# Optimization experiments

Measured on AMD Instinct MI355X. Metric: run time of the kernel, lower is better.

Reference implementation:

```python
import jax, jax.numpy as jnp
import numpy as np

HIDDEN = 1024
HEADS = 16
HEAD_DIM = HIDDEN // HEADS  # 64; softmax scale uses head_dim per SeqAttention(hidden_size=head_dim)


def setup_inputs() -> dict:
    key = jax.random.key(0)
    ks = jax.random.split(key, 7)
    B, M = 2, 2048
    s = 1.0 / np.sqrt(HIDDEN)
    return {
        "query": jax.random.normal(ks[0], (B, M, HIDDEN), jnp.float32),
        "key": jax.random.normal(ks[1], (B, M, HIDDEN), jnp.float32),
        "value": jax.random.normal(ks[2], (B, M, HIDDEN), jnp.float32),
        "Wq": jax.random.normal(ks[3], (HIDDEN, HIDDEN), jnp.float32) * s,
        "Wk": jax.random.normal(ks[4], (HIDDEN, HIDDEN), jnp.float32) * s,
        "Wv": jax.random.normal(ks[5], (HIDDEN, HIDDEN), jnp.float32) * s,
        "Wo": jax.random.normal(ks[6], (HIDDEN, HIDDEN), jnp.float32) * s,
    }


def _split_heads(x):
    # [B, T, H*D] -> [B, H, T, D]
    B, T, _ = x.shape
    return x.reshape(B, T, HEADS, HEAD_DIM).transpose(0, 2, 1, 3)


def reference(query, key, value, Wq, Wk, Wv, Wo):
    # nn.Linear(bias=False): y = x @ W.T
    q = _split_heads(query @ Wq.T)  # [B,H,M,D]
    k = _split_heads(key @ Wk.T)    # [B,H,N,D]
    v = _split_heads(value @ Wv.T)  # [B,H,N,D]
    scale = 1.0 / jnp.sqrt(jnp.asarray(HEAD_DIM, q.dtype))
    attn = jnp.einsum("bhmd,bhnd->bhmn", q, k) * scale
    attn = jax.nn.softmax(attn, axis=-1)
    out = jnp.einsum("bhmn,bhnd->bhmd", attn, v)  # [B,H,M,D]
    B, H, M, D = out.shape
    out = out.transpose(0, 2, 1, 3).reshape(B, M, H * D)
    return out @ Wo.T
```

## Files before the change

kernel.cpp:

```cpp
#include <hip/hip_runtime.h>

typedef __bf16 bf16;
typedef __bf16 bf16x2 __attribute__((ext_vector_type(2)));
typedef __bf16 bf16x8 __attribute__((ext_vector_type(8)));
typedef float  f32x4  __attribute__((ext_vector_type(4)));
typedef float  f32x16 __attribute__((ext_vector_type(16)));
typedef unsigned int u32;
typedef unsigned int u32x4 __attribute__((ext_vector_type(4)));

typedef __attribute__((address_space(1))) unsigned int gu32;
typedef __attribute__((address_space(3))) unsigned int lu32;

__device__ __forceinline__ void llds16(const void* g, void* l) {
  __builtin_amdgcn_global_load_lds((gu32*)g, (lu32*)l, 16, 0, 0);
}

__device__ __forceinline__ void cvt8(const float* __restrict__ src,
                                     bf16* __restrict__ dst, int i) {
  const float4* s4 = (const float4*)src;
  float4 a = s4[i * 2 + 0];
  float4 c = s4[i * 2 + 1];
  bf16x8 o;
  o[0] = (bf16)a.x; o[1] = (bf16)a.y; o[2] = (bf16)a.z; o[3] = (bf16)a.w;
  o[4] = (bf16)c.x; o[5] = (bf16)c.y; o[6] = (bf16)c.z; o[7] = (bf16)c.w;
  ((bf16x8*)dst)[i] = o;
}

__global__ __launch_bounds__(256) void cvt_bf16(const float* __restrict__ src,
                                                bf16* __restrict__ dst, int n8) {
  int i = blockIdx.x * blockDim.x + threadIdx.x;
  if (i < n8) cvt8(src, dst, i);
}

__global__ __launch_bounds__(256) void cvt_all(const float* __restrict__ w0,
                                               const float* __restrict__ w1,
                                               const float* __restrict__ w2,
                                               const float* __restrict__ w3,
                                               const float* __restrict__ x0,
                                               const float* __restrict__ x1,
                                               const float* __restrict__ x2,
                                               bf16* __restrict__ wdst,
                                               bf16* __restrict__ xdst) {
  const int b = blockIdx.x;
  if (b < 2048) {
    const int which = b >> 9;
    const float* src = (which == 0) ? w0 : (which == 1) ? w1 : (which == 2) ? w2 : w3;
    const int i = (b & 511) * 256 + threadIdx.x;
    cvt8(src, wdst + (size_t)which * (1u << 20), i);
  } else {
    const int b2 = b - 2048;
    const int which = b2 >> 11;
    const float* src = (which == 0) ? x0 : (which == 1) ? x1 : x2;
    const int i = (b2 & 2047) * 256 + threadIdx.x;
    cvt8(src, xdst + (size_t)which * (4u << 20), i);
  }
}

__global__ __launch_bounds__(256) void gemm_qkv(const bf16* __restrict__ A0,
                                                const bf16* __restrict__ A1,
                                                const bf16* __restrict__ A2,
                                                const bf16* __restrict__ Wb,
                                                bf16* __restrict__ qb,
                                                bf16* __restrict__ kb,
                                                bf16* __restrict__ vb,
                                                int zoff) {
  constexpr int K = 1024, BM = 128, BN = 128, BK = 32, NT = K / BK;
  __shared__ bf16 Alds[2][BM * BK];
  __shared__ bf16 Blds[2][BN * BK];
  const int t = threadIdx.x, w = t >> 6, l = t & 63;
  const int lr = l & 15, lg = l >> 4;
  const int bm = blockIdx.x * BM, bn = blockIdx.y * BN;
  const int z = blockIdx.z + zoff;
  const bf16* A = (z == 0) ? A0 : (z == 1) ? A1 : A2;
  const bf16* W = Wb + (size_t)z * (1u << 20);
  const int wm = (w >> 1) * 64, wn = (w & 1) * 64;

  f32x4 acc[4][4] = {};

  auto stage = [&](int buf, int kt) {
    const int k0 = kt * BK;
#pragma unroll
    for (int i = 0; i < 2; ++i) {
      int idx = i * 256 + t;
      int row = idx >> 2, kb2 = (idx & 3) * 16;
      llds16((const char*)A + ((size_t)(bm + row) * K + k0) * 2 + kb2,
             (char*)(&Alds[buf][0]) + (i * 4 + w) * 1024);
    }
#pragma unroll
    for (int i = 0; i < 2; ++i) {
      int idx = i * 256 + t;
      int row = idx >> 2, kb2 = (idx & 3) * 16;
      llds16((const char*)W + ((size_t)(bn + row) * K + k0) * 2 + kb2,
             (char*)(&Blds[buf][0]) + (i * 4 + w) * 1024);
    }
  };

  stage(0, 0);
  for (int kt = 0; kt < NT; ++kt) {
    __syncthreads();
    if (kt + 1 < NT) stage((kt + 1) & 1, kt + 1);
    const int cur = kt & 1;
    bf16x8 af[4], bfr[4];
#pragma unroll
    for (int i = 0; i < 4; ++i)
      af[i] = *(const bf16x8*)(&Alds[cur][(wm + i * 16 + lr) * BK + lg * 8]);
#pragma unroll
    for (int j = 0; j < 4; ++j)
      bfr[j] = *(const bf16x8*)(&Blds[cur][(wn + j * 16 + lr) * BK + lg * 8]);
    __builtin_amdgcn_s_setprio(1);
#pragma unroll
    for (int i = 0; i < 4; ++i)
#pragma unroll
      for (int j = 0; j < 4; ++j)
        acc[i][j] = __builtin_amdgcn_mfma_f32_16x16x32_bf16(af[i], bfr[j], acc[i][j], 0, 0, 0);
    __builtin_amdgcn_s_setprio(0);
  }

  bf16* Cout = (z == 0) ? qb : (z == 1) ? kb : vb;
  const float osc = (z == 0) ? 0.1803368801f : 1.0f;
#pragma unroll
  for (int i = 0; i < 4; ++i) {
#pragma unroll
    for (int j = 0; j < 4; ++j) {
#pragma unroll
      for (int r = 0; r < 4; ++r) {
        const int gm = bm + wm + i * 16 + lg * 4 + r;
        const int n  = bn + wn + j * 16 + lr;
        const int b = gm >> 11, m = gm & 2047;
        const int h = n >> 6, d = n & 63;
        const size_t off = (z < 2)
            ? ((size_t)((b * 16 + h) * 2048 + m) * 64 + d)
            : ((size_t)((b * 16 + h) * 64 + d) * 2048 + m);
        Cout[off] = (bf16)(acc[i][j][r] * osc);
      }
    }
  }
}

__global__ __launch_bounds__(256) void gemm_out(const bf16* __restrict__ A,
                                                const bf16* __restrict__ Bw,
                                                float* __restrict__ Cout) {
  constexpr int N = 1024, K = 1024;
  constexpr int BM = 128, BN = 64, BK = 32;
  __shared__ bf16 Alds[2][BM * BK];
  __shared__ bf16 Blds[2][BN * BK];
  const int t = threadIdx.x;
  const int w = t >> 6, l = t & 63;
  const int lr = l & 15, lg = l >> 4;
  const int bm = blockIdx.x * BM, bn = blockIdx.y * BN;
  const int wm = (w >> 1) * 64, wn = (w & 1) * 32;

  f32x4 acc[4][2] = {};

  auto stage = [&](int buf, int kt) {
    const int k0 = kt * BK;
#pragma unroll
    for (int i = 0; i < 2; ++i) {
      int idx = i * 256 + t;
      int row = idx >> 2, kb = (idx & 3) * 16;
      const char* g = (const char*)A + ((size_t)(bm + row) * K + k0) * 2 + kb;
      llds16(g, (char*)(&Alds[buf][0]) + (i * 4 + w) * 1024);
    }
    {
      int row = t >> 2, kb = (t & 3) * 16;
      const char* g = (const char*)Bw + ((size_t)(bn + row) * K + k0) * 2 + kb;
      llds16(g, (char*)(&Blds[buf][0]) + w * 1024);
    }
  };

  stage(0, 0);
  constexpr int NT = K / BK;
  for (int kt = 0; kt < NT; ++kt) {
    __syncthreads();
    if (kt + 1 < NT) stage((kt + 1) & 1, kt + 1);
    const int cur = kt & 1;
    bf16x8 af[4], bfr[2];
#pragma unroll
    for (int i = 0; i < 4; ++i)
      af[i] = *(const bf16x8*)(&Alds[cur][(wm + i * 16 + lr) * BK + lg * 8]);
#pragma unroll
    for (int j = 0; j < 2; ++j)
      bfr[j] = *(const bf16x8*)(&Blds[cur][(wn + j * 16 + lr) * BK + lg * 8]);
    __builtin_amdgcn_s_setprio(1);
#pragma unroll
    for (int i = 0; i < 4; ++i)
#pragma unroll
      for (int j = 0; j < 2; ++j)
        acc[i][j] = __builtin_amdgcn_mfma_f32_16x16x32_bf16(af[i], bfr[j], acc[i][j], 0, 0, 0);
    __builtin_amdgcn_s_setprio(0);
  }

#pragma unroll
  for (int i = 0; i < 4; ++i)
#pragma unroll
    for (int j = 0; j < 2; ++j)
#pragma unroll
      for (int r = 0; r < 4; ++r) {
        const int gm = bm + wm + i * 16 + lg * 4 + r;
        const int n  = bn + wn + j * 16 + lr;
        Cout[(size_t)gm * N + n] = acc[i][j][r];
      }
}

__global__ __launch_bounds__(256) void attn_fwd(const bf16* __restrict__ Qb,
                                                const bf16* __restrict__ Kb,
                                                const bf16* __restrict__ Vt,
                                                bf16* __restrict__ Out) {
  constexpr int Mlen = 2048, KVB = 64, NTT = Mlen / KVB;
  __shared__ bf16 Klds[3][KVB * 64];
  __shared__ bf16 Vlds[3][64 * KVB];
  const int t = threadIdx.x, w = t >> 6, l = t & 63;
  const int l31 = l & 31, hi = l >> 5;
  const int orig = blockIdx.x;
  const int wg = (orig & 7) * 64 + (orig >> 3);
  const int bh = wg >> 4;
  const int qr = (wg & 15) * 128 + w * 32;
  const int key = (l31 & 7) << 4;

  const bf16* qbase = Qb + ((size_t)bh * Mlen + qr + l31) * 64;
  bf16x8 qf[4];
#pragma unroll
  for (int dks = 0; dks < 4; ++dks)
    qf[dks] = *(const bf16x8*)(qbase + dks * 16 + hi * 8);

  f32x16 acco0 = {}, acco1 = {};
  float lsum = 0.f;

  const char* kTile0 = (const char*)Kb + (size_t)bh * Mlen * 64 * 2;
  const char* vBase  = (const char*)Vt + (size_t)bh * 64 * Mlen * 2;

  auto stageKV = [&](int buf, int tile) {
    const int kv0 = tile * KVB;
#pragma unroll
    for (int i = 0; i < 2; ++i) {
      int idx = i * 256 + t;
      int L = idx * 16;
      int row = L >> 7;
      int inner = (L & 127) ^ ((row & 7) << 4);
      llds16(kTile0 + (size_t)(kv0 + row) * 128 + inner,
             (char*)(&Klds[buf][0]) + (i * 4 + w) * 1024);
    }
#pragma unroll
    for (int i = 0; i < 2; ++i) {
      int idx = i * 256 + t;
      int L = idx * 16;
      int d = L >> 7;
      int inner = (L & 127) ^ ((d & 7) << 4);
      llds16(vBase + (size_t)d * (Mlen * 2) + kv0 * 2 + inner,
             (char*)(&Vlds[buf][0]) + (i * 4 + w) * 1024);
    }
  };

  stageKV(0, 0);
  int bufc = 0;
  for (int tile = 0; tile < NTT; ++tile) {
    const int bufn = (bufc == 2) ? 0 : bufc + 1;
    if (tile + 1 < NTT) {
      stageKV(bufn, tile + 1);
      asm volatile("s_waitcnt vmcnt(4)" ::: "memory");
    } else {
      asm volatile("s_waitcnt vmcnt(0)" ::: "memory");
    }
    __builtin_amdgcn_s_barrier();
    __builtin_amdgcn_sched_barrier(0);
    const char* kb_ = (const char*)(&Klds[bufc][0]);
    const char* vb_ = (const char*)(&Vlds[bufc][0]);

    f32x16 s0 = {}, s1 = {};
    __builtin_amdgcn_s_setprio(1);
#pragma unroll
    for (int dks = 0; dks < 4; ++dks) {
      const int a0 = (0 * 32 + l31) * 128 + ((dks * 32 + hi * 16) ^ key);
      const int a1 = (1 * 32 + l31) * 128 + ((dks * 32 + hi * 16) ^ key);
      bf16x8 kf0 = *(const bf16x8*)(kb_ + a0);
      bf16x8 kf1 = *(const bf16x8*)(kb_ + a1);
      s0 = __builtin_amdgcn_mfma_f32_32x32x16_bf16(kf0, qf[dks], s0, 0, 0, 0);
      s1 = __builtin_amdgcn_mfma_f32_32x32x16_bf16(kf1, qf[dks], s1, 0, 0, 0);
    }
    __builtin_amdgcn_s_setprio(0);

    u32 wrd0[8], wrd1[8];
    float ts = 0.f;
#pragma unroll
    for (int e2 = 0; e2 < 8; ++e2) {
      const float p00 = __builtin_amdgcn_exp2f(s0[2 * e2]);
      const float p01 = __builtin_amdgcn_exp2f(s0[2 * e2 + 1]);
      const float p10 = __builtin_amdgcn_exp2f(s1[2 * e2]);
      const float p11 = __builtin_amdgcn_exp2f(s1[2 * e2 + 1]);
      ts += (p00 + p01) + (p10 + p11);
      bf16x2 k0; k0[0] = (bf16)p00; k0[1] = (bf16)p01;
      bf16x2 k1; k1[0] = (bf16)p10; k1[1] = (bf16)p11;
      wrd0[e2] = __builtin_bit_cast(u32, k0);
      wrd1[e2] = __builtin_bit_cast(u32, k1);
    }
    lsum += ts;

    __builtin_amdgcn_s_setprio(1);
#pragma unroll
    for (int ks = 0; ks < 2; ++ks) {
      auto sa0 = __builtin_amdgcn_permlane32_swap(wrd0[4 * ks + 0], wrd0[4 * ks + 2], false, false);
      auto sa1 = __builtin_amdgcn_permlane32_swap(wrd0[4 * ks + 1], wrd0[4 * ks + 3], false, false);
      auto sb0 = __builtin_amdgcn_permlane32_swap(wrd1[4 * ks + 0], wrd1[4 * ks + 2], false, false);
      auto sb1 = __builtin_amdgcn_permlane32_swap(wrd1[4 * ks + 1], wrd1[4 * ks + 3], false, false);
      u32x4 fa, fb;
      fa[0] = (u32)sa0[0]; fa[1] = (u32)sa1[0]; fa[2] = (u32)sa0[1]; fa[3] = (u32)sa1[1];
      fb[0] = (u32)sb0[0]; fb[1] = (u32)sb1[0]; fb[2] = (u32)sb0[1]; fb[3] = (u32)sb1[1];
      const bf16x8 pa = __builtin_bit_cast(bf16x8, fa);
      const bf16x8 pb = __builtin_bit_cast(bf16x8, fb);
      const int c0 = (ks * 32 + hi * 16);
      bf16x8 va0 = *(const bf16x8*)(vb_ + (0 * 32 + l31) * 128 + ((0 * 64 + c0) ^ key));
      bf16x8 va1 = *(const bf16x8*)(vb_ + (1 * 32 + l31) * 128 + ((0 * 64 + c0) ^ key));
      bf16x8 vb0 = *(const bf16x8*)(vb_ + (0 * 32 + l31) * 128 + ((1 * 64 + c0) ^ key));
      bf16x8 vb1 = *(const bf16x8*)(vb_ + (1 * 32 + l31) * 128 + ((1 * 64 + c0) ^ key));
      acco0 = __builtin_amdgcn_mfma_f32_32x32x16_bf16(pa, va0, acco0, 0, 0, 0);
      acco1 = __builtin_amdgcn_mfma_f32_32x32x16_bf16(pa, va1, acco1, 0, 0, 0);
      acco0 = __builtin_amdgcn_mfma_f32_32x32x16_bf16(pb, vb0, acco0, 0, 0, 0);
      acco1 = __builtin_amdgcn_mfma_f32_32x32x16_bf16(pb, vb1, acco1, 0, 0, 0);
    }
    __builtin_amdgcn_s_setprio(0);
    bufc = bufn;
  }

  float lf = lsum + __shfl_xor(lsum, 32, 64);
  const float inv = 1.0f / lf;
  const int b = bh >> 4, h = bh & 15;
#pragma unroll
  for (int e = 0; e < 16; ++e) {
    const int ql = (e & 3) + 8 * (e >> 2) + 4 * hi;
    const float iv = __shfl(inv, ql, 64);
    const size_t row = (size_t)(b * 2048 + qr + ql) * 1024 + h * 64;
    Out[row + l31]      = (bf16)(acco0[e] * iv);
    Out[row + 32 + l31] = (bf16)(acco1[e] * iv);
  }
}

extern "C" void kernel_launch(void* const* d_in, const int* in_sizes, int n_in,
                              void* d_out, int out_size, void* d_ws, size_t ws_size,
                              hipStream_t stream) {
  const float* q  = (const float*)d_in[0];
  const float* k  = (const float*)d_in[1];
  const float* v  = (const float*)d_in[2];
  const float* Wq = (const float*)d_in[3];
  const float* Wk = (const float*)d_in[4];
  const float* Wv = (const float*)d_in[5];
  const float* Wo = (const float*)d_in[6];

  char* ws = (char*)d_ws;
  const dim3 cb(256);

  if (ws_size >= ((size_t)56 << 20)) {
    bf16* Wb = (bf16*)ws;
    bf16* Xq = (bf16*)(ws + (8u  << 20));
    bf16* Xk = (bf16*)(ws + (16u << 20));
    bf16* Xv = (bf16*)(ws + (24u << 20));
    bf16* qb = (bf16*)(ws + (32u << 20));
    bf16* kb = (bf16*)(ws + (40u << 20));
    bf16* vb = (bf16*)(ws + (48u << 20));
    bf16* Xa = (bf16*)(ws + (8u  << 20));

    cvt_all<<<8192, cb, 0, stream>>>(Wq, Wk, Wv, Wo, q, k, v, Wb, Xq);
    gemm_qkv<<<dim3(32, 8, 3), cb, 0, stream>>>(Xq, Xk, Xv, Wb, qb, kb, vb, 0);
    attn_fwd<<<512, cb, 0, stream>>>(qb, kb, vb, Xa);
    gemm_out<<<dim3(32, 16), cb, 0, stream>>>(Xa, Wb + 3 * (1u << 20), (float*)d_out);
  } else {
    bf16* Wb = (bf16*)ws;
    bf16* X  = (bf16*)(ws + (8u  << 20));
    bf16* qb = (bf16*)(ws + (16u << 20));
    bf16* kb = (bf16*)(ws + (24u << 20));
    bf16* vb = (bf16*)(ws + (32u << 20));
    bf16* Xa = (bf16*)(ws + (8u  << 20));

    cvt_all<<<2048, cb, 0, stream>>>(Wq, Wk, Wv, Wo, q, k, v, Wb, Wb);
    cvt_bf16<<<2048, cb, 0, stream>>>(q, X, 524288);
    gemm_qkv<<<dim3(32, 8, 1), cb, 0, stream>>>(X, X, X, Wb, qb, kb, vb, 0);
    cvt_bf16<<<2048, cb, 0, stream>>>(k, X, 524288);
    gemm_qkv<<<dim3(32, 8, 1), cb, 0, stream>>>(X, X, X, Wb, qb, kb, vb, 1);
    cvt_bf16<<<2048, cb, 0, stream>>>(v, X, 524288);
    gemm_qkv<<<dim3(32, 8, 1), cb, 0, stream>>>(X, X, X, Wb, qb, kb, vb, 2);
    attn_fwd<<<512, cb, 0, stream>>>(qb, kb, vb, Xa);
    gemm_out<<<dim3(32, 16), cb, 0, stream>>>(Xa, Wb + 3 * (1u << 20), (float*)d_out);
  }
}
```

Before: 131.8 us.

## Widen output GEMM tile to 128x128 and compute softmax row sums via MFMA

The output projection GEMM moves from a 128x64 to a 128x128 block tile: each wave now holds a 4x4 set of accumulators and the grid is halved to 32x8 blocks. This increases reuse of A and B per LDS load but leaves fewer blocks to occupy the GPU. In attention, the per-lane scalar exp accumulation and the cross-lane shuffle of the row sum are replaced by an extra MFMA that multiplies P by a ones vector, so the row sums come out in the same layout as the output accumulator. This removes VALU adds and shuffles in exchange for two more MFMAs per iteration and 16 more accumulator registers. The row sums are now taken from the bf16-rounded probabilities rather than the fp32 values.

```diff
diff --git a/kernel.cpp b/kernel.cpp
--- a/kernel.cpp
+++ b/kernel.cpp
@@ -141,16 +141,16 @@
                                                 const bf16* __restrict__ Bw,
                                                 float* __restrict__ Cout) {
   constexpr int N = 1024, K = 1024;
-  constexpr int BM = 128, BN = 64, BK = 32;
+  constexpr int BM = 128, BN = 128, BK = 32, NT = K / BK;
   __shared__ bf16 Alds[2][BM * BK];
   __shared__ bf16 Blds[2][BN * BK];
   const int t = threadIdx.x;
   const int w = t >> 6, l = t & 63;
   const int lr = l & 15, lg = l >> 4;
   const int bm = blockIdx.x * BM, bn = blockIdx.y * BN;
-  const int wm = (w >> 1) * 64, wn = (w & 1) * 32;
-
-  f32x4 acc[4][2] = {};
+  const int wm = (w >> 1) * 64, wn = (w & 1) * 64;
+
+  f32x4 acc[4][4] = {};
 
   auto stage = [&](int buf, int kt) {
     const int k0 = kt * BK;
@@ -158,34 +158,35 @@
     for (int i = 0; i < 2; ++i) {
       int idx = i * 256 + t;
       int row = idx >> 2, kb = (idx & 3) * 16;
-      const char* g = (const char*)A + ((size_t)(bm + row) * K + k0) * 2 + kb;
-      llds16(g, (char*)(&Alds[buf][0]) + (i * 4 + w) * 1024);
-    }
-    {
-      int row = t >> 2, kb = (t & 3) * 16;
-      const char* g = (const char*)Bw + ((size_t)(bn + row) * K + k0) * 2 + kb;
-      llds16(g, (char*)(&Blds[buf][0]) + w * 1024);
+      llds16((const char*)A + ((size_t)(bm + row) * K + k0) * 2 + kb,
+             (char*)(&Alds[buf][0]) + (i * 4 + w) * 1024);
+    }
+#pragma unroll
+    for (int i = 0; i < 2; ++i) {
+      int idx = i * 256 + t;
+      int row = idx >> 2, kb = (idx & 3) * 16;
+      llds16((const char*)Bw + ((size_t)(bn + row) * K + k0) * 2 + kb,
+             (char*)(&Blds[buf][0]) + (i * 4 + w) * 1024);
     }
   };
 
   stage(0, 0);
-  constexpr int NT = K / BK;
   for (int kt = 0; kt < NT; ++kt) {
     __syncthreads();
     if (kt + 1 < NT) stage((kt + 1) & 1, kt + 1);
     const int cur = kt & 1;
-    bf16x8 af[4], bfr[2];
+    bf16x8 af[4], bfr[4];
 #pragma unroll
     for (int i = 0; i < 4; ++i)
       af[i] = *(const bf16x8*)(&Alds[cur][(wm + i * 16 + lr) * BK + lg * 8]);
 #pragma unroll
-    for (int j = 0; j < 2; ++j)
+    for (int j = 0; j < 4; ++j)
       bfr[j] = *(const bf16x8*)(&Blds[cur][(wn + j * 16 + lr) * BK + lg * 8]);
     __builtin_amdgcn_s_setprio(1);
 #pragma unroll
     for (int i = 0; i < 4; ++i)
 #pragma unroll
-      for (int j = 0; j < 2; ++j)
+      for (int j = 0; j < 4; ++j)
         acc[i][j] = __builtin_amdgcn_mfma_f32_16x16x32_bf16(af[i], bfr[j], acc[i][j], 0, 0, 0);
     __builtin_amdgcn_s_setprio(0);
   }
@@ -193,7 +194,7 @@
 #pragma unroll
   for (int i = 0; i < 4; ++i)
 #pragma unroll
-    for (int j = 0; j < 2; ++j)
+    for (int j = 0; j < 4; ++j)
 #pragma unroll
       for (int r = 0; r < 4; ++r) {
         const int gm = bm + wm + i * 16 + lg * 4 + r;
@@ -223,8 +224,13 @@
   for (int dks = 0; dks < 4; ++dks)
     qf[dks] = *(const bf16x8*)(qbase + dks * 16 + hi * 8);
 
+  u32x4 onesw;
+  onesw[0] = 0x3F803F80u; onesw[1] = 0x3F803F80u;
+  onesw[2] = 0x3F803F80u; onesw[3] = 0x3F803F80u;
+  const bf16x8 ones = __builtin_bit_cast(bf16x8, onesw);
+
   f32x16 acco0 = {}, acco1 = {};
-  float lsum = 0.f;
+  f32x16 accl = {};
 
   const char* kTile0 = (const char*)Kb + (size_t)bh * Mlen * 64 * 2;
   const char* vBase  = (const char*)Vt + (size_t)bh * 64 * Mlen * 2;
@@ -280,20 +286,17 @@
     __builtin_amdgcn_s_setprio(0);
 
     u32 wrd0[8], wrd1[8];
-    float ts = 0.f;
 #pragma unroll
     for (int e2 = 0; e2 < 8; ++e2) {
       const float p00 = __builtin_amdgcn_exp2f(s0[2 * e2]);
       const float p01 = __builtin_amdgcn_exp2f(s0[2 * e2 + 1]);
       const float p10 = __builtin_amdgcn_exp2f(s1[2 * e2]);
       const float p11 = __builtin_amdgcn_exp2f(s1[2 * e2 + 1]);
-      ts += (p00 + p01) + (p10 + p11);
       bf16x2 k0; k0[0] = (bf16)p00; k0[1] = (bf16)p01;
       bf16x2 k1; k1[0] = (bf16)p10; k1[1] = (bf16)p11;
       wrd0[e2] = __builtin_bit_cast(u32, k0);
       wrd1[e2] = __builtin_bit_cast(u32, k1);
     }
-    lsum += ts;
 
     __builtin_amdgcn_s_setprio(1);
 #pragma unroll
@@ -314,20 +317,20 @@
       bf16x8 vb1 = *(const bf16x8*)(vb_ + (1 * 32 + l31) * 128 + ((1 * 64 + c0) ^ key));
       acco0 = __builtin_amdgcn_mfma_f32_32x32x16_bf16(pa, va0, acco0, 0, 0, 0);
       acco1 = __builtin_amdgcn_mfma_f32_32x32x16_bf16(pa, va1, acco1, 0, 0, 0);
+      accl  = __builtin_amdgcn_mfma_f32_32x32x16_bf16(pa, ones, accl, 0, 0, 0);
       acco0 = __builtin_amdgcn_mfma_f32_32x32x16_bf16(pb, vb0, acco0, 0, 0, 0);
       acco1 = __builtin_amdgcn_mfma_f32_32x32x16_bf16(pb, vb1, acco1, 0, 0, 0);
+      accl  = __builtin_amdgcn_mfma_f32_32x32x16_bf16(pb, ones, accl, 0, 0, 0);
     }
     __builtin_amdgcn_s_setprio(0);
     bufc = bufn;
   }
 
-  float lf = lsum + __shfl_xor(lsum, 32, 64);
-  const float inv = 1.0f / lf;
   const int b = bh >> 4, h = bh & 15;
 #pragma unroll
   for (int e = 0; e < 16; ++e) {
     const int ql = (e & 3) + 8 * (e >> 2) + 4 * hi;
-    const float iv = __shfl(inv, ql, 64);
+    const float iv = 1.0f / accl[e];
     const size_t row = (size_t)(b * 2048 + qr + ql) * 1024 + h * 64;
     Out[row + l31]      = (bf16)(acco0[e] * iv);
     Out[row + 32 + l31] = (bf16)(acco1[e] * iv);
@@ -361,7 +364,7 @@
     cvt_all<<<8192, cb, 0, stream>>>(Wq, Wk, Wv, Wo, q, k, v, Wb, Xq);
     gemm_qkv<<<dim3(32, 8, 3), cb, 0, stream>>>(Xq, Xk, Xv, Wb, qb, kb, vb, 0);
     attn_fwd<<<512, cb, 0, stream>>>(qb, kb, vb, Xa);
-    gemm_out<<<dim3(32, 16), cb, 0, stream>>>(Xa, Wb + 3 * (1u << 20), (float*)d_out);
+    gemm_out<<<dim3(32, 8), cb, 0, stream>>>(Xa, Wb + 3 * (1u << 20), (float*)d_out);
   } else {
     bf16* Wb = (bf16*)ws;
     bf16* X  = (bf16*)(ws + (8u  << 20));
@@ -378,6 +381,6 @@
     cvt_bf16<<<2048, cb, 0, stream>>>(v, X, 524288);
     gemm_qkv<<<dim3(32, 8, 1), cb, 0, stream>>>(X, X, X, Wb, qb, kb, vb, 2);
     attn_fwd<<<512, cb, 0, stream>>>(qb, kb, vb, Xa);
-    gemm_out<<<dim3(32, 16), cb, 0, stream>>>(Xa, Wb + 3 * (1u << 20), (float*)d_out);
-  }
-}
+    gemm_out<<<dim3(32, 8), cb, 0, stream>>>(Xa, Wb + 3 * (1u << 20), (float*)d_out);
+  }
+}
```

After: 134.0 us. About the same (+1.7%).
